# Performance work log

Measured on AMD Instinct MI355X. Metric: run time of the kernel, lower is better.

## Reference

```python
import jax, jax.numpy as jnp
import numpy as np

T_CONST = 0.1

def _hardtanh(w):
    # F.hardtanh(w, min_val=1e-10, max_val=1)
    return jnp.clip(w, 1e-10, 1.0)

def _forward(inp, hn, w_str2str, w_str2snr, w_m12m1, w_m12str, w_thal2m1,
             w_m12thal, w_thal2str, w_str2stn, w_stn2snr, w_snr2thal,
             str2str_fixed, inp_weight, mean_w, mean_b, std_w, std_b, hid_dim):
    H = hid_dim
    H5 = 5 * H
    Z = jnp.zeros((H, H), dtype=inp.dtype)
    n_inhib = int(0.3 * H)

    # Diagonal 'D' matrices realized as column scalings (D is diagonal)
    m12m1_d = jnp.concatenate([jnp.ones((H - n_inhib,)), -jnp.ones((n_inhib,))])

    # Block masks
    str2str_mask = jnp.zeros((H, H))
    m12str_mask = jnp.concatenate([jnp.ones((H, H - n_inhib)), jnp.zeros((H, n_inhib))], axis=1)
    str2stn_mask = jnp.concatenate([jnp.zeros((H, H // 2)), jnp.ones((H, H // 2))], axis=1)
    str2snr_mask = jnp.concatenate([jnp.ones((H, H // 2)), jnp.zeros((H, H // 2))], axis=1)

    # Region masks over the full 5H state
    thal_mask = jnp.concatenate([jnp.zeros((3 * H,)), jnp.ones((H,)), jnp.zeros((H,))])
    m1_mask = jnp.zeros((H5,))  # cat(zeros(4H), zeros(H)) in the source

    # Effective recurrent blocks (str2str_D = stn2snr_D = snr2thal_D = str2snr_D = -I)
    str2str_rec = -(str2str_mask * _hardtanh(w_str2str) + str2str_fixed)
    m12m1_rec = _hardtanh(w_m12m1) * m12m1_d[None, :]
    m12str_rec = m12str_mask * _hardtanh(w_m12str)
    str2snr_rec = -(str2snr_mask * _hardtanh(w_str2snr))
    thal2m1_rec = _hardtanh(w_thal2m1)
    m12thal_rec = _hardtanh(w_m12thal)
    thal2str_rec = _hardtanh(w_thal2str)
    str2stn_rec = str2stn_mask * _hardtanh(w_str2stn)
    stn2snr_rec = -_hardtanh(w_str2stn)  # NOTE: source uses str2stn weight here (faithful to original)
    snr2thal_rec = -_hardtanh(w_snr2thal)

    W_rec = jnp.concatenate([
        jnp.concatenate([str2str_rec, Z, Z, thal2str_rec, m12str_rec], axis=1),
        jnp.concatenate([str2stn_rec, Z, Z, Z, Z], axis=1),
        jnp.concatenate([str2snr_rec, stn2snr_rec, Z, Z, Z], axis=1),
        jnp.concatenate([Z, Z, snr2thal_rec, Z, m12thal_rec], axis=1),
        jnp.concatenate([Z, Z, Z, thal2m1_rec, m12m1_rec], axis=1),
    ], axis=0)  # [5H, 5H]

    # Precompute masked input drive for all timesteps: [T, B, 5H]
    u = jnp.einsum('bti,ih->tbh', inp, _hardtanh(inp_weight)) * thal_mask

    W_rec_T = W_rec.T

    def step(h, u_t):
        # (W_rec @ h.T).T == h @ W_rec.T
        h_new = jax.nn.relu((1.0 - T_CONST) * h + T_CONST * (h @ W_rec_T + u_t))
        return h_new, h_new

    _, hs = jax.lax.scan(step, hn[0], u)  # hs: [T, B, 5H]
    rnn_out = jnp.transpose(hs, (1, 0, 2))  # [B, T, 5H]
    hn_last = rnn_out[:, -1, :][None]  # [1, B, 5H]

    masked = rnn_out * m1_mask
    mean_out = masked @ mean_w + mean_b
    std_out = jnp.clip(masked @ std_w + std_b, -5.0, 10.0)
    return mean_out, std_out, rnn_out, hn_last


def setup_inputs() -> dict:
    H, B, T, I, A = 256, 64, 512, 4, 1
    H5 = 5 * H
    key = jax.random.key(0)
    ks = jax.random.split(key, 20)
    u01 = lambda k, shape, s: jax.random.uniform(k, shape, dtype=jnp.float32) * s
    inputs = {
        'inp': jax.random.uniform(ks[0], (B, T, I), dtype=jnp.float32),
        'hn': jnp.zeros((1, B, H5), dtype=jnp.float32),
        'w_str2str': u01(ks[1], (H, H), 0.01),
        'w_str2snr': u01(ks[2], (H, H), 0.01),
        'w_m12m1': u01(ks[3], (H, H), 0.01),
        'w_m12str': u01(ks[4], (H, H), 0.01),
        'w_thal2m1': u01(ks[5], (H, H), 0.01),
        'w_m12thal': u01(ks[6], (H, H), 0.01),
        'w_thal2str': u01(ks[7], (H, H), 0.01),
        'w_str2stn': u01(ks[8], (H, H), 0.01),
        'w_stn2snr': u01(ks[9], (H, H), 0.01),
        'w_snr2thal': u01(ks[10], (H, H), 0.01),
        'inp_weight': u01(ks[12], (I, H5), 0.1),
        'mean_w': jax.random.normal(ks[13], (H5, A), dtype=jnp.float32) * 0.02,
        'mean_b': jnp.zeros((A,), dtype=jnp.float32),
        'std_w': jax.random.normal(ks[14], (H5, A), dtype=jnp.float32) * 0.02,
        'std_b': jnp.zeros((A,), dtype=jnp.float32),
        'hid_dim': H,
    }
    keep = jax.random.bernoulli(ks[11], 0.15, (H, H)).astype(jnp.float32)
    inputs['str2str_fixed'] = u01(ks[15], (H, H), 0.01) * keep
    return inputs


def reference(inp, hn, w_str2str, w_str2snr, w_m12m1, w_m12str, w_thal2m1,
              w_m12thal, w_thal2str, w_str2stn, w_stn2snr, w_snr2thal,
              str2str_fixed, inp_weight, mean_w, mean_b, std_w, std_b, hid_dim):
    return _forward(inp, hn, w_str2str, w_str2snr, w_m12m1, w_m12str, w_thal2m1,
                    w_m12thal, w_thal2str, w_str2stn, w_stn2snr, w_snr2thal,
                    str2str_fixed, inp_weight, mean_w, mean_b, std_w, std_b, hid_dim)
```

## Files before the change

kernel.cpp:

```cpp
#include <hip/hip_runtime.h>

typedef unsigned short u16;
typedef unsigned long long u64;
typedef unsigned u32;
typedef __bf16 v8bf __attribute__((ext_vector_type(8)));
typedef float f32x4 __attribute__((ext_vector_type(4)));
typedef u16 u16x4 __attribute__((ext_vector_type(4)));
typedef u32 u32x4 __attribute__((ext_vector_type(4)));
typedef u32 u32x2 __attribute__((ext_vector_type(2)));

#define H5 1280
#define TT 512
#define NBLK 80
#define SPL 81920

#define OFF_W0 0
#define OFF_W1 3276800
#define OFF_W2 6553600
#define OFF_HS 9830400
#define OFF_WIN 10813440
#define OFF_CNT 10817536

#define MFMA(a, b, c) __builtin_amdgcn_mfma_f32_16x16x32_bf16(a, b, c, 0, 0, 0)

__device__ __forceinline__ float htanh_(float x) {
  return fminf(fmaxf(x, 1e-10f), 1.0f);
}
__device__ __forceinline__ u16 f2b(float f) {
  unsigned u = __float_as_uint(f);
  return (u16)((u + 0x7fffu + ((u >> 16) & 1u)) >> 16);
}
__device__ __forceinline__ float b2f(u16 b) {
  return __uint_as_float(((unsigned)b) << 16);
}
__device__ __forceinline__ u32 umin_(u32 a, u32 b) { return a < b ? a : b; }

__device__ __forceinline__ void st8_sc1(u16* p, u16x4 v) {
  union { u16x4 s; u64 q; } u;
  u.s = v;
  asm volatile("global_store_dwordx2 %0, %1, off sc1" :: "v"(p), "v"(u.q) : "memory");
}

__global__ void build_w(const float* __restrict__ w_str2snr, const float* __restrict__ w_m12m1,
                        const float* __restrict__ w_m12str, const float* __restrict__ w_thal2m1,
                        const float* __restrict__ w_m12thal, const float* __restrict__ w_thal2str,
                        const float* __restrict__ w_str2stn, const float* __restrict__ w_snr2thal,
                        const float* __restrict__ fixedw, u16* __restrict__ W0,
                        u16* __restrict__ W1, u16* __restrict__ W2) {
  int idx = blockIdx.x * 256 + threadIdx.x;
  if (idx >= H5 * H5) return;
  int j = idx / H5, k = idx - j * H5;
  int jr = j >> 8, kr = k >> 8, kk = k & 255;
  int o = (j & 255) * 256 + kk;
  float w = 0.0f;
  if (jr == 0) {
    if (kr == 0) w = -fixedw[o];
    else if (kr == 3) w = htanh_(w_thal2str[o]);
    else if (kr == 4) w = (kk < 180) ? htanh_(w_m12str[o]) : 0.0f;
  } else if (jr == 1) {
    if (kr == 0) w = (kk >= 128) ? htanh_(w_str2stn[o]) : 0.0f;
  } else if (jr == 2) {
    if (kr == 0) w = (kk < 128) ? -htanh_(w_str2snr[o]) : 0.0f;
    else if (kr == 1) w = -htanh_(w_str2stn[o]);
  } else if (jr == 3) {
    if (kr == 2) w = -htanh_(w_snr2thal[o]);
    else if (kr == 4) w = htanh_(w_m12thal[o]);
  } else {
    if (kr == 3) w = htanh_(w_thal2m1[o]);
    else if (kr == 4) w = (kk < 180) ? htanh_(w_m12m1[o]) : -htanh_(w_m12m1[o]);
  }
  u16 c0 = f2b(w);  float r1 = w - b2f(c0);
  u16 c1 = f2b(r1); float r2 = r1 - b2f(c1);
  u16 c2 = f2b(r2);
  W0[idx] = c0; W1[idx] = c1; W2[idx] = c2;
}

__global__ void build_misc(const float* __restrict__ hn, const float* __restrict__ inp_weight,
                           const float* __restrict__ mean_b, const float* __restrict__ std_b,
                           float* __restrict__ out, u16* __restrict__ hs, float* __restrict__ Win) {
  int gid = blockIdx.x * 256 + threadIdx.x;
  if (gid < 65536) {
    out[gid] = (gid < 32768) ? mean_b[0] : fminf(10.0f, fmaxf(-5.0f, std_b[0]));
  } else if (gid < 65536 + SPL) {
    int i = gid - 65536;
    float v = hn[i];
    u16 c0 = f2b(v);  float r1 = v - b2f(c0);
    u16 c1 = f2b(r1); float r2 = r1 - b2f(c1);
    u16 c2 = f2b(r2);
    hs[i] = c0; hs[SPL + i] = c1; hs[2 * SPL + i] = c2;
  } else if (gid < 65536 + SPL + 1024) {
    int i = gid - 65536 - SPL;
    Win[i] = htanh_(inp_weight[(i >> 8) * H5 + 768 + (i & 255)]);
  }
}

template <int R> struct RC;
template <> struct RC<0> { static constexpr int kb[3] = {0, 768, 1024}; static constexpr int nch[3] = {8, 8, 8}; };
template <> struct RC<1> { static constexpr int kb[3] = {128, 0, 0};    static constexpr int nch[3] = {4, 0, 0}; };
template <> struct RC<2> { static constexpr int kb[3] = {0, 256, 0};    static constexpr int nch[3] = {4, 8, 0}; };
template <> struct RC<3> { static constexpr int kb[3] = {512, 1024, 0}; static constexpr int nch[3] = {8, 8, 0}; };
template <> struct RC<4> { static constexpr int kb[3] = {768, 1024, 0}; static constexpr int nch[3] = {8, 8, 0}; };

template <int R>
__device__ __forceinline__ void stage_h(const u16* __restrict__ hs_r, int bcol0,
                                        u16* __restrict__ sm) {
  v8bf regs[9];
  int n = 0;
#pragma unroll
  for (int q = 0; q < 3; ++q) {
    if (RC<R>::nch[q] > 0) {
      const int span8 = RC<R>::nch[q] * 4;
      const int units = span8 * 24;
      const int rounds = (units + 255) / 256;
#pragma unroll
      for (int r = 0; r < rounds; ++r) {
        int u = threadIdx.x + r * 256;
        if (u < units) {
          int kunit = u & (span8 - 1);
          int sc = u / span8;
          int split = sc >> 3, col = sc & 7;
          const u16* gp = hs_r + split * SPL + (long)(bcol0 + col) * H5 +
                          RC<R>::kb[q] + kunit * 8;
          asm volatile("global_load_dwordx4 %0, %1, off sc1"
                       : "=v"(regs[n]) : "v"(gp) : "memory");
        }
        ++n;
      }
    }
  }
  asm volatile("s_waitcnt vmcnt(0)" ::: "memory");
  __builtin_amdgcn_sched_barrier(0);
  n = 0;
  int base = 0;
#pragma unroll
  for (int q = 0; q < 3; ++q) {
    if (RC<R>::nch[q] > 0) {
      const int span8 = RC<R>::nch[q] * 4;
      const int colstride = RC<R>::nch[q] * 32 + 8;
      const int units = span8 * 24;
      const int rounds = (units + 255) / 256;
#pragma unroll
      for (int r = 0; r < rounds; ++r) {
        int u = threadIdx.x + r * 256;
        if (u < units) {
          int kunit = u & (span8 - 1);
          int sc = u / span8;
          *(v8bf*)(sm + base + sc * colstride + kunit * 8) = regs[n];
        }
        ++n;
      }
      base += 24 * colstride;
    }
  }
}

template <int R>
__device__ __forceinline__ void mm_lds(const u16* __restrict__ sm, int lk, int col,
                                       const u16* __restrict__ W0, const u16* __restrict__ W1,
                                       const u16* __restrict__ W2, long jrowA, long jrowB,
                                       f32x4 (&out)[2]) {
  f32x4 acc[2][6];
#pragma unroll
  for (int t = 0; t < 2; ++t)
#pragma unroll
    for (int s = 0; s < 6; ++s) acc[t][s] = {0.f, 0.f, 0.f, 0.f};
  int base = 0;
#pragma unroll
  for (int q = 0; q < 3; ++q) {
    if (RC<R>::nch[q] > 0) {
      const int kbq = RC<R>::kb[q];
      const int colstride = RC<R>::nch[q] * 32 + 8;
#pragma unroll
      for (int c = 0; c < RC<R>::nch[q]; ++c) {
        v8bf B0 = *(const v8bf*)(sm + base + (0 * 8 + col) * colstride + c * 32 + lk);
        v8bf B1 = *(const v8bf*)(sm + base + (1 * 8 + col) * colstride + c * 32 + lk);
        v8bf B2 = *(const v8bf*)(sm + base + (2 * 8 + col) * colstride + c * 32 + lk);
        long oA = jrowA + kbq + c * 32, oB = jrowB + kbq + c * 32;
        v8bf a0 = *(const v8bf*)(W0 + oA);
        v8bf a1 = *(const v8bf*)(W1 + oA);
        v8bf a2 = *(const v8bf*)(W2 + oA);
        v8bf b0 = *(const v8bf*)(W0 + oB);
        v8bf b1 = *(const v8bf*)(W1 + oB);
        v8bf b2 = *(const v8bf*)(W2 + oB);
        acc[0][0] = MFMA(a0, B0, acc[0][0]);
        acc[1][0] = MFMA(b0, B0, acc[1][0]);
        acc[0][1] = MFMA(a0, B1, acc[0][1]);
        acc[1][1] = MFMA(b0, B1, acc[1][1]);
        acc[0][2] = MFMA(a0, B2, acc[0][2]);
        acc[1][2] = MFMA(b0, B2, acc[1][2]);
        acc[0][3] = MFMA(a1, B0, acc[0][3]);
        acc[1][3] = MFMA(b1, B0, acc[1][3]);
        acc[0][4] = MFMA(a1, B1, acc[0][4]);
        acc[1][4] = MFMA(b1, B1, acc[1][4]);
        acc[0][5] = MFMA(a2, B0, acc[0][5]);
        acc[1][5] = MFMA(b2, B0, acc[1][5]);
      }
      base += 24 * colstride;
    }
  }
#pragma unroll
  for (int t = 0; t < 2; ++t)
#pragma unroll
    for (int rr = 0; rr < 4; ++rr)
      out[t][rr] = ((acc[t][0][rr] + acc[t][3][rr]) + (acc[t][1][rr] + acc[t][4][rr])) +
                   (acc[t][2][rr] + acc[t][5][rr]);
}

template <int R>
__device__ void pers_loop(int j0, int bcol, bool act, int hi, int lk, int lr, int bcol0,
                          const float* __restrict__ inp_b, const float* __restrict__ hn,
                          const u16* __restrict__ W0, const u16* __restrict__ W1,
                          const u16* __restrict__ W2, u16* __restrict__ hs,
                          float* __restrict__ rnn_b, float* __restrict__ hn_last,
                          const float* __restrict__ Win, u32* __restrict__ flags, int slot,
                          u16* __restrict__ sm) {
  const long jrowA = (long)(j0 + lr) * H5 + lk;
  const long jrowB = (long)(j0 + 16 + lr) * H5 + lk;
  const int col = lr & 7;

  float wA[4][4], wB[4][4];
  if constexpr (R == 3) {
#pragma unroll
    for (int i = 0; i < 4; ++i)
#pragma unroll
      for (int rr = 0; rr < 4; ++rr) {
        wA[i][rr] = Win[i * 256 + (j0 - 768) + hi * 4 + rr];
        wB[i][rr] = Win[i * 256 + (j0 - 768 + 16) + hi * 4 + rr];
      }
  }

  f32x4 hpA, hpB;
  {
    const float* ha = hn + (long)bcol * H5 + j0 + hi * 4;
#pragma unroll
    for (int rr = 0; rr < 4; ++rr) { hpA[rr] = ha[rr]; hpB[rr] = ha[16 + rr]; }
  }

  for (int t = 0; t < TT; ++t) {
    const u16* hs_r = hs + (t & 1) * (3 * SPL);
    u16* hs_w = hs + ((t & 1) ^ 1) * (3 * SPL);

    stage_h<R>(hs_r, bcol0, sm);
    __syncthreads();

    f32x4 o[2];
    mm_lds<R>(sm, lk, col, W0, W1, W2, jrowA, jrowB, o);

    if constexpr (R == 3) {
      const float* ip = inp_b + t * 4;
      float i0 = ip[0], i1 = ip[1], i2 = ip[2], i3 = ip[3];
#pragma unroll
      for (int rr = 0; rr < 4; ++rr) {
        o[0][rr] += i0 * wA[0][rr] + i1 * wA[1][rr] + i2 * wA[2][rr] + i3 * wA[3][rr];
        o[1][rr] += i0 * wB[0][rr] + i1 * wB[1][rr] + i2 * wB[2][rr] + i3 * wB[3][rr];
      }
    }

    f32x4 hA, hB;
#pragma unroll
    for (int rr = 0; rr < 4; ++rr) {
      hA[rr] = fmaxf(0.0f, 0.9f * hpA[rr] + 0.1f * o[0][rr]);
      hB[rr] = fmaxf(0.0f, 0.9f * hpB[rr] + 0.1f * o[1][rr]);
    }
    hpA = hA; hpB = hB;

    if (act) {
      float* rp = rnn_b + (long)t * H5 + j0 + hi * 4;
      *(f32x4*)rp = hA;
      *(f32x4*)(rp + 16) = hB;
    }

    if (t < TT - 1) {
      if (act) {
        u16x4 sA0, sA1, sA2, sB0, sB1, sB2;
#pragma unroll
        for (int rr = 0; rr < 4; ++rr) {
          float v = hA[rr];
          u16 c0 = f2b(v);  float r1 = v - b2f(c0);
          u16 c1 = f2b(r1); float r2 = r1 - b2f(c1);
          sA0[rr] = c0; sA1[rr] = c1; sA2[rr] = f2b(r2);
          v = hB[rr];
          c0 = f2b(v);  r1 = v - b2f(c0);
          c1 = f2b(r1); r2 = r1 - b2f(c1);
          sB0[rr] = c0; sB1[rr] = c1; sB2[rr] = f2b(r2);
        }
        u16* hw = hs_w + (long)bcol * H5 + j0 + hi * 4;
        st8_sc1(hw, sA0);
        st8_sc1(hw + SPL, sA1);
        st8_sc1(hw + 2 * SPL, sA2);
        st8_sc1(hw + 16, sB0);
        st8_sc1(hw + 16 + SPL, sB1);
        st8_sc1(hw + 16 + 2 * SPL, sB2);
      }
      asm volatile("s_waitcnt vmcnt(0)" ::: "memory");
      __syncthreads();
      if (threadIdx.x == 0) {
        u32 tv = (u32)(t + 1);
        u32* myf = flags + slot;
        asm volatile("global_store_dword %0, %1, off sc1" :: "v"(myf), "v"(tv) : "memory");
        for (;;) {
          u32x4 f0, f1; u32x2 f2;
          asm volatile("global_load_dwordx4 %0, %1, off sc1" : "=v"(f0) : "v"(flags) : "memory");
          asm volatile("global_load_dwordx4 %0, %1, off sc1" : "=v"(f1) : "v"(flags + 4) : "memory");
          asm volatile("global_load_dwordx2 %0, %1, off sc1" : "=v"(f2) : "v"(flags + 8) : "memory");
          asm volatile("s_waitcnt vmcnt(0)" ::: "memory");
          u32 m = umin_(umin_(umin_(f0[0], f0[1]), umin_(f0[2], f0[3])),
                        umin_(umin_(f1[0], f1[1]), umin_(f1[2], f1[3])));
          m = umin_(m, umin_(f2[0], f2[1]));
          if (m >= tv) break;
          __builtin_amdgcn_s_sleep(1);
        }
      }
      __syncthreads();
    } else if (act) {
      float* hl = hn_last + (long)bcol * H5 + j0 + hi * 4;
      *(f32x4*)hl = hA;
      *(f32x4*)(hl + 16) = hB;
    }
  }
}

__global__ void __launch_bounds__(256, 1)
rnn_pers(const float* __restrict__ inp, const float* __restrict__ hn,
         const u16* __restrict__ W0, const u16* __restrict__ W1, const u16* __restrict__ W2,
         u16* __restrict__ hs, float* __restrict__ rnn, float* __restrict__ hn_last,
         const float* __restrict__ Win, u32* __restrict__ cnt) {
  __shared__ u16 smh[19008];
  const int tid = threadIdx.x, bx = blockIdx.x;
  const int g = bx & 7, slot = bx >> 3;
  const int lane = tid & 63, w = tid >> 6;
  const int lr = lane & 15, hi = lane >> 4, lk = hi * 8;
  const int bcol0 = g * 8;
  const int bcol = bcol0 + (lr & 7);
  const bool act = lr < 8;
  const int j0 = slot * 128 + w * 32;
  u32* flags = cnt + 128 + g * 32;
  float* rnn_b = rnn + (long)bcol * TT * H5;
  const float* inp_b = inp + (long)bcol * TT * 4;
  switch (slot >> 1) {
    case 0: pers_loop<0>(j0, bcol, act, hi, lk, lr, bcol0, inp_b, hn, W0, W1, W2, hs, rnn_b, hn_last, Win, flags, slot, smh); break;
    case 1: pers_loop<1>(j0, bcol, act, hi, lk, lr, bcol0, inp_b, hn, W0, W1, W2, hs, rnn_b, hn_last, Win, flags, slot, smh); break;
    case 2: pers_loop<2>(j0, bcol, act, hi, lk, lr, bcol0, inp_b, hn, W0, W1, W2, hs, rnn_b, hn_last, Win, flags, slot, smh); break;
    case 3: pers_loop<3>(j0, bcol, act, hi, lk, lr, bcol0, inp_b, hn, W0, W1, W2, hs, rnn_b, hn_last, Win, flags, slot, smh); break;
    default: pers_loop<4>(j0, bcol, act, hi, lk, lr, bcol0, inp_b, hn, W0, W1, W2, hs, rnn_b, hn_last, Win, flags, slot, smh); break;
  }
}

template <int R>
__device__ void step_one(int t, int j0, int bcol, bool act, int hi, int lk, int lr,
                         const float* __restrict__ inp_b, const float* __restrict__ hn,
                         const u16* __restrict__ W0, const u16* __restrict__ W1,
                         const u16* __restrict__ W2, u16* __restrict__ hs,
                         float* __restrict__ rnn, float* __restrict__ rnn_b,
                         float* __restrict__ hn_last, const float* __restrict__ Win) {
  const long jrowA = (long)(j0 + lr) * H5 + lk;
  const long jrowB = (long)(j0 + 16 + lr) * H5 + lk;
  const u16* hs_r = hs + (t & 1) * (3 * SPL);
  u16* hs_w = hs + ((t & 1) ^ 1) * (3 * SPL);

  f32x4 acc[2][6];
#pragma unroll
  for (int tt = 0; tt < 2; ++tt)
#pragma unroll
    for (int s = 0; s < 6; ++s) acc[tt][s] = {0.f, 0.f, 0.f, 0.f};
#pragma unroll
  for (int q = 0; q < 3; ++q) {
    if (RC<R>::nch[q] > 0) {
      const int kbq = RC<R>::kb[q];
      const u16* hb = hs_r + (long)bcol * H5 + kbq + lk;
#pragma unroll
      for (int c = 0; c < RC<R>::nch[q]; ++c) {
        v8bf B0 = *(const v8bf*)(hb + c * 32);
        v8bf B1 = *(const v8bf*)(hb + SPL + c * 32);
        v8bf B2 = *(const v8bf*)(hb + 2 * SPL + c * 32);
        long oA = jrowA + kbq + c * 32, oB = jrowB + kbq + c * 32;
        v8bf a0 = *(const v8bf*)(W0 + oA);
        v8bf a1 = *(const v8bf*)(W1 + oA);
        v8bf a2 = *(const v8bf*)(W2 + oA);
        v8bf b0 = *(const v8bf*)(W0 + oB);
        v8bf b1 = *(const v8bf*)(W1 + oB);
        v8bf b2 = *(const v8bf*)(W2 + oB);
        acc[0][0] = MFMA(a0, B0, acc[0][0]);
        acc[1][0] = MFMA(b0, B0, acc[1][0]);
        acc[0][1] = MFMA(a0, B1, acc[0][1]);
        acc[1][1] = MFMA(b0, B1, acc[1][1]);
        acc[0][2] = MFMA(a0, B2, acc[0][2]);
        acc[1][2] = MFMA(b0, B2, acc[1][2]);
        acc[0][3] = MFMA(a1, B0, acc[0][3]);
        acc[1][3] = MFMA(b1, B0, acc[1][3]);
        acc[0][4] = MFMA(a1, B1, acc[0][4]);
        acc[1][4] = MFMA(b1, B1, acc[1][4]);
        acc[0][5] = MFMA(a2, B0, acc[0][5]);
        acc[1][5] = MFMA(b2, B0, acc[1][5]);
      }
    }
  }
  f32x4 o[2];
#pragma unroll
  for (int tt = 0; tt < 2; ++tt)
#pragma unroll
    for (int rr = 0; rr < 4; ++rr)
      o[tt][rr] = ((acc[tt][0][rr] + acc[tt][3][rr]) + (acc[tt][1][rr] + acc[tt][4][rr])) +
                  (acc[tt][2][rr] + acc[tt][5][rr]);

  if constexpr (R == 3) {
    const float* ip = inp_b + t * 4;
    float i0 = ip[0], i1 = ip[1], i2 = ip[2], i3 = ip[3];
#pragma unroll
    for (int rr = 0; rr < 4; ++rr) {
      o[0][rr] += i0 * Win[0 * 256 + (j0 - 768) + hi * 4 + rr] +
                  i1 * Win[1 * 256 + (j0 - 768) + hi * 4 + rr] +
                  i2 * Win[2 * 256 + (j0 - 768) + hi * 4 + rr] +
                  i3 * Win[3 * 256 + (j0 - 768) + hi * 4 + rr];
      o[1][rr] += i0 * Win[0 * 256 + (j0 - 768 + 16) + hi * 4 + rr] +
                  i1 * Win[1 * 256 + (j0 - 768 + 16) + hi * 4 + rr] +
                  i2 * Win[2 * 256 + (j0 - 768 + 16) + hi * 4 + rr] +
                  i3 * Win[3 * 256 + (j0 - 768 + 16) + hi * 4 + rr];
    }
  }

  f32x4 hpA, hpB;
  {
    const float* ha = (t == 0) ? (hn + (long)bcol * H5 + j0 + hi * 4)
                               : (rnn + ((long)bcol * TT + (t - 1)) * H5 + j0 + hi * 4);
#pragma unroll
    for (int rr = 0; rr < 4; ++rr) { hpA[rr] = ha[rr]; hpB[rr] = ha[16 + rr]; }
  }
  f32x4 hA, hB;
#pragma unroll
  for (int rr = 0; rr < 4; ++rr) {
    hA[rr] = fmaxf(0.0f, 0.9f * hpA[rr] + 0.1f * o[0][rr]);
    hB[rr] = fmaxf(0.0f, 0.9f * hpB[rr] + 0.1f * o[1][rr]);
  }
  if (act) {
    float* rp = rnn_b + (long)t * H5 + j0 + hi * 4;
    *(f32x4*)rp = hA;
    *(f32x4*)(rp + 16) = hB;
    if (t < TT - 1) {
      u16x4 sA0, sA1, sA2, sB0, sB1, sB2;
#pragma unroll
      for (int rr = 0; rr < 4; ++rr) {
        float v = hA[rr];
        u16 c0 = f2b(v);  float r1 = v - b2f(c0);
        u16 c1 = f2b(r1); float r2 = r1 - b2f(c1);
        sA0[rr] = c0; sA1[rr] = c1; sA2[rr] = f2b(r2);
        v = hB[rr];
        c0 = f2b(v);  r1 = v - b2f(c0);
        c1 = f2b(r1); r2 = r1 - b2f(c1);
        sB0[rr] = c0; sB1[rr] = c1; sB2[rr] = f2b(r2);
      }
      u16* hw = hs_w + (long)bcol * H5 + j0 + hi * 4;
      *(u64*)hw = *(u64*)&sA0;
      *(u64*)(hw + SPL) = *(u64*)&sA1;
      *(u64*)(hw + 2 * SPL) = *(u64*)&sA2;
      *(u64*)(hw + 16) = *(u64*)&sB0;
      *(u64*)(hw + 16 + SPL) = *(u64*)&sB1;
      *(u64*)(hw + 16 + 2 * SPL) = *(u64*)&sB2;
    } else {
      float* hl = hn_last + (long)bcol * H5 + j0 + hi * 4;
      *(f32x4*)hl = hA;
      *(f32x4*)(hl + 16) = hB;
    }
  }
}

__global__ void __launch_bounds__(256, 1)
rnn_step(const float* __restrict__ inp, const float* __restrict__ hn,
         const u16* __restrict__ W0, const u16* __restrict__ W1, const u16* __restrict__ W2,
         u16* __restrict__ hs, float* __restrict__ rnn, float* __restrict__ hn_last,
         const float* __restrict__ Win, int t) {
  const int tid = threadIdx.x, bx = blockIdx.x;
  const int g = bx & 7, slot = bx >> 3;
  const int lane = tid & 63, w = tid >> 6;
  const int lr = lane & 15, hi = lane >> 4, lk = hi * 8;
  const int bcol = g * 8 + (lr & 7);
  const bool act = lr < 8;
  const int j0 = slot * 128 + w * 32;
  float* rnn_b = rnn + (long)bcol * TT * H5;
  const float* inp_b = inp + (long)bcol * TT * 4;
  switch (slot >> 1) {
    case 0: step_one<0>(t, j0, bcol, act, hi, lk, lr, inp_b, hn, W0, W1, W2, hs, rnn, rnn_b, hn_last, Win); break;
    case 1: step_one<1>(t, j0, bcol, act, hi, lk, lr, inp_b, hn, W0, W1, W2, hs, rnn, rnn_b, hn_last, Win); break;
    case 2: step_one<2>(t, j0, bcol, act, hi, lk, lr, inp_b, hn, W0, W1, W2, hs, rnn, rnn_b, hn_last, Win); break;
    case 3: step_one<3>(t, j0, bcol, act, hi, lk, lr, inp_b, hn, W0, W1, W2, hs, rnn, rnn_b, hn_last, Win); break;
    default: step_one<4>(t, j0, bcol, act, hi, lk, lr, inp_b, hn, W0, W1, W2, hs, rnn, rnn_b, hn_last, Win); break;
  }
}

extern "C" void kernel_launch(void* const* d_in, const int* in_sizes, int n_in,
                              void* d_out, int out_size, void* d_ws, size_t ws_size,
                              hipStream_t stream) {
  const float* inp        = (const float*)d_in[0];
  const float* hn         = (const float*)d_in[1];
  const float* w_str2snr  = (const float*)d_in[3];
  const float* w_m12m1    = (const float*)d_in[4];
  const float* w_m12str   = (const float*)d_in[5];
  const float* w_thal2m1  = (const float*)d_in[6];
  const float* w_m12thal  = (const float*)d_in[7];
  const float* w_thal2str = (const float*)d_in[8];
  const float* w_str2stn  = (const float*)d_in[9];
  const float* w_snr2thal = (const float*)d_in[11];
  const float* inp_weight = (const float*)d_in[12];
  const float* mean_b     = (const float*)d_in[14];
  const float* std_b      = (const float*)d_in[16];
  const float* fixedw     = (const float*)d_in[18];

  char* ws = (char*)d_ws;
  u16* W0 = (u16*)(ws + OFF_W0);
  u16* W1 = (u16*)(ws + OFF_W1);
  u16* W2 = (u16*)(ws + OFF_W2);
  u16* hsb = (u16*)(ws + OFF_HS);
  float* Win = (float*)(ws + OFF_WIN);
  u32* cnt = (u32*)(ws + OFF_CNT);

  float* out = (float*)d_out;
  float* rnn = out + 65536;
  float* hnl = out + 65536 + 41943040;

  build_w<<<6400, 256, 0, stream>>>(w_str2snr, w_m12m1, w_m12str, w_thal2m1, w_m12thal,
                                    w_thal2str, w_str2stn, w_snr2thal, fixedw, W0, W1, W2);
  build_misc<<<581, 256, 0, stream>>>(hn, inp_weight, mean_b, std_b, out, hsb, Win);

  bool coop_ok = (ws_size >= (size_t)OFF_CNT + 2048);
  hipError_t e = hipErrorUnknown;
  if (coop_ok) {
    hipMemsetAsync(cnt, 0, 1536, stream);
    void* args[] = {(void*)&inp, (void*)&hn, (void*)&W0, (void*)&W1, (void*)&W2, (void*)&hsb,
                    (void*)&rnn, (void*)&hnl, (void*)&Win, (void*)&cnt};
    e = hipLaunchCooperativeKernel((const void*)rnn_pers, dim3(NBLK), dim3(256),
                                   args, 0, stream);
  }
  if (e != hipSuccess) {
    for (int t = 0; t < TT; ++t)
      rnn_step<<<NBLK, 256, 0, stream>>>(inp, hn, W0, W1, W2, hsb, rnn, hnl, Win, t);
  }
}
```

Measured before the change: 10.39 ms.

## Drop LDS staging of hidden state and parallelize flag barrier polling

Removes the shared-memory staging of the hidden-state splits and the __syncthreads that followed it. Each wave now loads its B fragments straight from global memory with coherent sc1 loads, batched per segment before the MFMAs. The inter-block flag barrier now uses one wave: each lane polls one flag with an atomic-add-of-zero and the wave combines them with __all, replacing a single thread that read every flag and took a min. This targets per-step sync and staging latency in the persistent recurrent loop, at the cost of redundant global loads across waves and extra register pressure from the B arrays.

```diff
diff --git a/kernel.cpp b/kernel.cpp
--- a/kernel.cpp
+++ b/kernel.cpp
@@ -6,8 +6,6 @@
 typedef __bf16 v8bf __attribute__((ext_vector_type(8)));
 typedef float f32x4 __attribute__((ext_vector_type(4)));
 typedef u16 u16x4 __attribute__((ext_vector_type(4)));
-typedef u32 u32x4 __attribute__((ext_vector_type(4)));
-typedef u32 u32x2 __attribute__((ext_vector_type(2)));
 
 #define H5 1280
 #define TT 512
@@ -33,7 +31,6 @@
 __device__ __forceinline__ float b2f(u16 b) {
   return __uint_as_float(((unsigned)b) << 16);
 }
-__device__ __forceinline__ u32 umin_(u32 a, u32 b) { return a < b ? a : b; }
 
 __device__ __forceinline__ void st8_sc1(u16* p, u16x4 v) {
   union { u16x4 s; u64 q; } u;
@@ -101,80 +98,40 @@
 template <> struct RC<3> { static constexpr int kb[3] = {512, 1024, 0}; static constexpr int nch[3] = {8, 8, 0}; };
 template <> struct RC<4> { static constexpr int kb[3] = {768, 1024, 0}; static constexpr int nch[3] = {8, 8, 0}; };
 
-template <int R>
-__device__ __forceinline__ void stage_h(const u16* __restrict__ hs_r, int bcol0,
-                                        u16* __restrict__ sm) {
-  v8bf regs[9];
-  int n = 0;
-#pragma unroll
-  for (int q = 0; q < 3; ++q) {
-    if (RC<R>::nch[q] > 0) {
-      const int span8 = RC<R>::nch[q] * 4;
-      const int units = span8 * 24;
-      const int rounds = (units + 255) / 256;
-#pragma unroll
-      for (int r = 0; r < rounds; ++r) {
-        int u = threadIdx.x + r * 256;
-        if (u < units) {
-          int kunit = u & (span8 - 1);
-          int sc = u / span8;
-          int split = sc >> 3, col = sc & 7;
-          const u16* gp = hs_r + split * SPL + (long)(bcol0 + col) * H5 +
-                          RC<R>::kb[q] + kunit * 8;
-          asm volatile("global_load_dwordx4 %0, %1, off sc1"
-                       : "=v"(regs[n]) : "v"(gp) : "memory");
-        }
-        ++n;
-      }
-    }
-  }
-  asm volatile("s_waitcnt vmcnt(0)" ::: "memory");
-  __builtin_amdgcn_sched_barrier(0);
-  n = 0;
-  int base = 0;
-#pragma unroll
-  for (int q = 0; q < 3; ++q) {
-    if (RC<R>::nch[q] > 0) {
-      const int span8 = RC<R>::nch[q] * 4;
-      const int colstride = RC<R>::nch[q] * 32 + 8;
-      const int units = span8 * 24;
-      const int rounds = (units + 255) / 256;
-#pragma unroll
-      for (int r = 0; r < rounds; ++r) {
-        int u = threadIdx.x + r * 256;
-        if (u < units) {
-          int kunit = u & (span8 - 1);
-          int sc = u / span8;
-          *(v8bf*)(sm + base + sc * colstride + kunit * 8) = regs[n];
-        }
-        ++n;
-      }
-      base += 24 * colstride;
-    }
-  }
-}
-
-template <int R>
-__device__ __forceinline__ void mm_lds(const u16* __restrict__ sm, int lk, int col,
-                                       const u16* __restrict__ W0, const u16* __restrict__ W1,
-                                       const u16* __restrict__ W2, long jrowA, long jrowB,
-                                       f32x4 (&out)[2]) {
+template <int R, int MODE>
+__device__ __forceinline__ void mm_step(const u16* __restrict__ hs_r, int bcol, int lk,
+                                        const u16* __restrict__ W0, const u16* __restrict__ W1,
+                                        const u16* __restrict__ W2, long jrowA, long jrowB,
+                                        f32x4 (&out)[2]) {
   f32x4 acc[2][6];
 #pragma unroll
   for (int t = 0; t < 2; ++t)
 #pragma unroll
     for (int s = 0; s < 6; ++s) acc[t][s] = {0.f, 0.f, 0.f, 0.f};
-  int base = 0;
 #pragma unroll
   for (int q = 0; q < 3; ++q) {
     if (RC<R>::nch[q] > 0) {
       const int kbq = RC<R>::kb[q];
-      const int colstride = RC<R>::nch[q] * 32 + 8;
+      const u16* hb = hs_r + (long)bcol * H5 + kbq + lk;
+      v8bf B0[8], B1[8], B2[8];
 #pragma unroll
       for (int c = 0; c < RC<R>::nch[q]; ++c) {
-        v8bf B0 = *(const v8bf*)(sm + base + (0 * 8 + col) * colstride + c * 32 + lk);
-        v8bf B1 = *(const v8bf*)(sm + base + (1 * 8 + col) * colstride + c * 32 + lk);
-        v8bf B2 = *(const v8bf*)(sm + base + (2 * 8 + col) * colstride + c * 32 + lk);
+        if constexpr (MODE == 0) {
+          asm volatile("global_load_dwordx4 %0, %1, off sc1" : "=v"(B0[c]) : "v"(hb + c * 32) : "memory");
+          asm volatile("global_load_dwordx4 %0, %1, off sc1" : "=v"(B1[c]) : "v"(hb + SPL + c * 32) : "memory");
+          asm volatile("global_load_dwordx4 %0, %1, off sc1" : "=v"(B2[c]) : "v"(hb + 2 * SPL + c * 32) : "memory");
+        } else {
+          B0[c] = *(const v8bf*)(hb + c * 32);
+          B1[c] = *(const v8bf*)(hb + SPL + c * 32);
+          B2[c] = *(const v8bf*)(hb + 2 * SPL + c * 32);
+        }
+      }
+      if constexpr (MODE == 0) {
+        asm volatile("s_waitcnt vmcnt(0)" ::: "memory");
+        __builtin_amdgcn_sched_barrier(0);
+      }
+#pragma unroll
+      for (int c = 0; c < RC<R>::nch[q]; ++c) {
         long oA = jrowA + kbq + c * 32, oB = jrowB + kbq + c * 32;
         v8bf a0 = *(const v8bf*)(W0 + oA);
         v8bf a1 = *(const v8bf*)(W1 + oA);
@@ -182,20 +139,19 @@
         v8bf b0 = *(const v8bf*)(W0 + oB);
         v8bf b1 = *(const v8bf*)(W1 + oB);
         v8bf b2 = *(const v8bf*)(W2 + oB);
-        acc[0][0] = MFMA(a0, B0, acc[0][0]);
-        acc[1][0] = MFMA(b0, B0, acc[1][0]);
-        acc[0][1] = MFMA(a0, B1, acc[0][1]);
-        acc[1][1] = MFMA(b0, B1, acc[1][1]);
-        acc[0][2] = MFMA(a0, B2, acc[0][2]);
-        acc[1][2] = MFMA(b0, B2, acc[1][2]);
-        acc[0][3] = MFMA(a1, B0, acc[0][3]);
-        acc[1][3] = MFMA(b1, B0, acc[1][3]);
-        acc[0][4] = MFMA(a1, B1, acc[0][4]);
-        acc[1][4] = MFMA(b1, B1, acc[1][4]);
-        acc[0][5] = MFMA(a2, B0, acc[0][5]);
-        acc[1][5] = MFMA(b2, B0, acc[1][5]);
-      }
-      base += 24 * colstride;
+        acc[0][0] = MFMA(a0, B0[c], acc[0][0]);
+        acc[1][0] = MFMA(b0, B0[c], acc[1][0]);
+        acc[0][1] = MFMA(a0, B1[c], acc[0][1]);
+        acc[1][1] = MFMA(b0, B1[c], acc[1][1]);
+        acc[0][2] = MFMA(a0, B2[c], acc[0][2]);
+        acc[1][2] = MFMA(b0, B2[c], acc[1][2]);
+        acc[0][3] = MFMA(a1, B0[c], acc[0][3]);
+        acc[1][3] = MFMA(b1, B0[c], acc[1][3]);
+        acc[0][4] = MFMA(a1, B1[c], acc[0][4]);
+        acc[1][4] = MFMA(b1, B1[c], acc[1][4]);
+        acc[0][5] = MFMA(a2, B0[c], acc[0][5]);
+        acc[1][5] = MFMA(b2, B0[c], acc[1][5]);
+      }
     }
   }
 #pragma unroll
@@ -207,16 +163,14 @@
 }
 
 template <int R>
-__device__ void pers_loop(int j0, int bcol, bool act, int hi, int lk, int lr, int bcol0,
+__device__ void pers_loop(int j0, int bcol, bool act, int hi, int lk, int lr,
                           const float* __restrict__ inp_b, const float* __restrict__ hn,
                           const u16* __restrict__ W0, const u16* __restrict__ W1,
                           const u16* __restrict__ W2, u16* __restrict__ hs,
                           float* __restrict__ rnn_b, float* __restrict__ hn_last,
-                          const float* __restrict__ Win, u32* __restrict__ flags, int slot,
-                          u16* __restrict__ sm) {
+                          const float* __restrict__ Win, u32* __restrict__ flags, int slot) {
   const long jrowA = (long)(j0 + lr) * H5 + lk;
   const long jrowB = (long)(j0 + 16 + lr) * H5 + lk;
-  const int col = lr & 7;
 
   float wA[4][4], wB[4][4];
   if constexpr (R == 3) {
@@ -240,11 +194,8 @@
     const u16* hs_r = hs + (t & 1) * (3 * SPL);
     u16* hs_w = hs + ((t & 1) ^ 1) * (3 * SPL);
 
-    stage_h<R>(hs_r, bcol0, sm);
-    __syncthreads();
-
     f32x4 o[2];
-    mm_lds<R>(sm, lk, col, W0, W1, W2, jrowA, jrowB, o);
+    mm_step<R, 0>(hs_r, bcol, lk, W0, W1, W2, jrowA, jrowB, o);
 
     if constexpr (R == 3) {
       const float* ip = inp_b + t * 4;
@@ -294,20 +245,26 @@
       }
       asm volatile("s_waitcnt vmcnt(0)" ::: "memory");
       __syncthreads();
-      if (threadIdx.x == 0) {
-        u32 tv = (u32)(t + 1);
-        u32* myf = flags + slot;
-        asm volatile("global_store_dword %0, %1, off sc1" :: "v"(myf), "v"(tv) : "memory");
+      if (threadIdx.x < 64) {
+        const int lane = threadIdx.x;
+        const u32 tv = (u32)(t + 1);
+        if (lane == slot) {
+          u32* myf = flags + slot;
+          asm volatile("global_store_dword %0, %1, off sc1" :: "v"(myf), "v"(tv) : "memory");
+        }
+        u32* pa = flags + (lane < 10 ? lane : 0);
         for (;;) {
-          u32x4 f0, f1; u32x2 f2;
-          asm volatile("global_load_dwordx4 %0, %1, off sc1" : "=v"(f0) : "v"(flags) : "memory");
-          asm volatile("global_load_dwordx4 %0, %1, off sc1" : "=v"(f1) : "v"(flags + 4) : "memory");
-          asm volatile("global_load_dwordx2 %0, %1, off sc1" : "=v"(f2) : "v"(flags + 8) : "memory");
-          asm volatile("s_waitcnt vmcnt(0)" ::: "memory");
-          u32 m = umin_(umin_(umin_(f0[0], f0[1]), umin_(f0[2], f0[3])),
-                        umin_(umin_(f1[0], f1[1]), umin_(f1[2], f1[3])));
-          m = umin_(m, umin_(f2[0], f2[1]));
-          if (m >= tv) break;
+          bool ok;
+          if (lane < 10) {
+            u32 ret;
+            asm volatile("global_atomic_add %0, %1, %2, off sc0 sc1\n\t"
+                         "s_waitcnt vmcnt(0)"
+                         : "=v"(ret) : "v"(pa), "v"(0u) : "memory");
+            ok = ret >= tv;
+          } else {
+            ok = true;
+          }
+          if (__all(ok)) break;
           __builtin_amdgcn_s_sleep(1);
         }
       }
@@ -325,24 +282,22 @@
          const u16* __restrict__ W0, const u16* __restrict__ W1, const u16* __restrict__ W2,
          u16* __restrict__ hs, float* __restrict__ rnn, float* __restrict__ hn_last,
          const float* __restrict__ Win, u32* __restrict__ cnt) {
-  __shared__ u16 smh[19008];
   const int tid = threadIdx.x, bx = blockIdx.x;
   const int g = bx & 7, slot = bx >> 3;
   const int lane = tid & 63, w = tid >> 6;
   const int lr = lane & 15, hi = lane >> 4, lk = hi * 8;
-  const int bcol0 = g * 8;
-  const int bcol = bcol0 + (lr & 7);
+  const int bcol = g * 8 + (lr & 7);
   const bool act = lr < 8;
   const int j0 = slot * 128 + w * 32;
   u32* flags = cnt + 128 + g * 32;
   float* rnn_b = rnn + (long)bcol * TT * H5;
   const float* inp_b = inp + (long)bcol * TT * 4;
   switch (slot >> 1) {
-    case 0: pers_loop<0>(j0, bcol, act, hi, lk, lr, bcol0, inp_b, hn, W0, W1, W2, hs, rnn_b, hn_last, Win, flags, slot, smh); break;
-    case 1: pers_loop<1>(j0, bcol, act, hi, lk, lr, bcol0, inp_b, hn, W0, W1, W2, hs, rnn_b, hn_last, Win, flags, slot, smh); break;
-    case 2: pers_loop<2>(j0, bcol, act, hi, lk, lr, bcol0, inp_b, hn, W0, W1, W2, hs, rnn_b, hn_last, Win, flags, slot, smh); break;
-    case 3: pers_loop<3>(j0, bcol, act, hi, lk, lr, bcol0, inp_b, hn, W0, W1, W2, hs, rnn_b, hn_last, Win, flags, slot, smh); break;
-    default: pers_loop<4>(j0, bcol, act, hi, lk, lr, bcol0, inp_b, hn, W0, W1, W2, hs, rnn_b, hn_last, Win, flags, slot, smh); break;
+    case 0: pers_loop<0>(j0, bcol, act, hi, lk, lr, inp_b, hn, W0, W1, W2, hs, rnn_b, hn_last, Win, flags, slot); break;
+    case 1: pers_loop<1>(j0, bcol, act, hi, lk, lr, inp_b, hn, W0, W1, W2, hs, rnn_b, hn_last, Win, flags, slot); break;
+    case 2: pers_loop<2>(j0, bcol, act, hi, lk, lr, inp_b, hn, W0, W1, W2, hs, rnn_b, hn_last, Win, flags, slot); break;
+    case 3: pers_loop<3>(j0, bcol, act, hi, lk, lr, inp_b, hn, W0, W1, W2, hs, rnn_b, hn_last, Win, flags, slot); break;
+    default: pers_loop<4>(j0, bcol, act, hi, lk, lr, inp_b, hn, W0, W1, W2, hs, rnn_b, hn_last, Win, flags, slot); break;
   }
 }
 
@@ -358,50 +313,8 @@
   const u16* hs_r = hs + (t & 1) * (3 * SPL);
   u16* hs_w = hs + ((t & 1) ^ 1) * (3 * SPL);
 
-  f32x4 acc[2][6];
-#pragma unroll
-  for (int tt = 0; tt < 2; ++tt)
-#pragma unroll
-    for (int s = 0; s < 6; ++s) acc[tt][s] = {0.f, 0.f, 0.f, 0.f};
-#pragma unroll
-  for (int q = 0; q < 3; ++q) {
-    if (RC<R>::nch[q] > 0) {
-      const int kbq = RC<R>::kb[q];
-      const u16* hb = hs_r + (long)bcol * H5 + kbq + lk;
-#pragma unroll
-      for (int c = 0; c < RC<R>::nch[q]; ++c) {
-        v8bf B0 = *(const v8bf*)(hb + c * 32);
-        v8bf B1 = *(const v8bf*)(hb + SPL + c * 32);
-        v8bf B2 = *(const v8bf*)(hb + 2 * SPL + c * 32);
-        long oA = jrowA + kbq + c * 32, oB = jrowB + kbq + c * 32;
-        v8bf a0 = *(const v8bf*)(W0 + oA);
-        v8bf a1 = *(const v8bf*)(W1 + oA);
-        v8bf a2 = *(const v8bf*)(W2 + oA);
-        v8bf b0 = *(const v8bf*)(W0 + oB);
-        v8bf b1 = *(const v8bf*)(W1 + oB);
-        v8bf b2 = *(const v8bf*)(W2 + oB);
-        acc[0][0] = MFMA(a0, B0, acc[0][0]);
-        acc[1][0] = MFMA(b0, B0, acc[1][0]);
-        acc[0][1] = MFMA(a0, B1, acc[0][1]);
-        acc[1][1] = MFMA(b0, B1, acc[1][1]);
-        acc[0][2] = MFMA(a0, B2, acc[0][2]);
-        acc[1][2] = MFMA(b0, B2, acc[1][2]);
-        acc[0][3] = MFMA(a1, B0, acc[0][3]);
-        acc[1][3] = MFMA(b1, B0, acc[1][3]);
-        acc[0][4] = MFMA(a1, B1, acc[0][4]);
-        acc[1][4] = MFMA(b1, B1, acc[1][4]);
-        acc[0][5] = MFMA(a2, B0, acc[0][5]);
-        acc[1][5] = MFMA(b2, B0, acc[1][5]);
-      }
-    }
-  }
   f32x4 o[2];
-#pragma unroll
-  for (int tt = 0; tt < 2; ++tt)
-#pragma unroll
-    for (int rr = 0; rr < 4; ++rr)
-      o[tt][rr] = ((acc[tt][0][rr] + acc[tt][3][rr]) + (acc[tt][1][rr] + acc[tt][4][rr])) +
-                  (acc[tt][2][rr] + acc[tt][5][rr]);
+  mm_step<R, 2>(hs_r, bcol, lk, W0, W1, W2, jrowA, jrowB, o);
 
   if constexpr (R == 3) {
     const float* ip = inp_b + t * 4;
```

Result: slower. 13.47 ms (+29.7%).
